# Performance work log

Measured on AMD Instinct MI355X. Metric: run time of the kernel, lower is better.

## Reference

```python
import jax, jax.numpy as jnp
import numpy as np
from jax import lax

D_MODEL = 768
D_INNER = 1536  # expand * dim
D_STATE = 16
D_CONV = 4
DEPTH = 12
IMG = 224
PATCH = 16
BATCH = 8
NUM_PATCHES = ((IMG - PATCH) // PATCH + 1) ** 2  # 196
L = NUM_PATCHES + 1  # 197 (cls token)
EPS = 1e-5


def setup_inputs() -> dict:
    key = jax.random.key(0)
    ks = jax.random.split(key, 16)
    s = 0.02  # trunc_normal std used by the torch module
    conv_std = np.sqrt(2.0 / (PATCH * PATCH * D_MODEL)).astype(np.float32)
    A = jnp.tile(jnp.log(jnp.arange(1, D_STATE + 1, dtype=jnp.float32)), (DEPTH, D_INNER, 1))
    return {
        "x": jax.random.normal(ks[0], (BATCH, 3, IMG, IMG), jnp.float32),
        "conv_w": jax.random.normal(ks[1], (D_MODEL, 3, PATCH, PATCH), jnp.float32) * conv_std,
        "conv_b": jnp.zeros((D_MODEL,), jnp.float32),
        "cls_token": jax.random.normal(ks[2], (1, 1, D_MODEL), jnp.float32) * s,
        "pos_embed": jax.random.normal(ks[3], (1, L, D_MODEL), jnp.float32) * s,
        "ln_w": jnp.ones((DEPTH, D_MODEL), jnp.float32),
        "ln_b": jnp.zeros((DEPTH, D_MODEL), jnp.float32),
        "in_proj_w": jax.random.normal(ks[4], (DEPTH, 2 * D_INNER, D_MODEL), jnp.float32) * s,
        "conv1d_w": jax.random.normal(ks[5], (DEPTH, D_INNER, 1, D_CONV), jnp.float32) * 0.25,
        "conv1d_b": jnp.zeros((DEPTH, D_INNER), jnp.float32),
        "x_proj_w": jax.random.normal(ks[6], (DEPTH, 2 * D_STATE, D_INNER), jnp.float32) * s,
        "dt_proj_w": jax.random.normal(ks[7], (DEPTH, D_INNER, D_INNER), jnp.float32) * s,
        "dt_proj_b": jnp.zeros((DEPTH, D_INNER), jnp.float32),
        "A_log": A,
        "D_param": jnp.ones((DEPTH, D_INNER), jnp.float32),
        "out_proj_w": jax.random.normal(ks[8], (DEPTH, D_MODEL, D_INNER), jnp.float32) * s,
        "norm_w": jnp.ones((D_MODEL,), jnp.float32),
        "norm_b": jnp.zeros((D_MODEL,), jnp.float32),
    }


def layernorm(x, w, b):
    m = jnp.mean(x, axis=-1, keepdims=True)
    v = jnp.mean(jnp.square(x - m), axis=-1, keepdims=True)
    return (x - m) * lax.rsqrt(v + EPS) * w + b


def mamba_block(x, in_w, cw, cb, xp_w, dt_w, dt_b, A_log, Dp, out_w):
    # x: (B, L, D_MODEL)
    Bn = x.shape[0]
    xz = jnp.einsum("bld,ed->ble", x, in_w)            # (B,L,2*di)
    xi, z = jnp.split(xz, 2, axis=-1)
    # depthwise causal conv1d (torch pads d_conv-1 both sides then truncates to L == left-pad only)
    xc = lax.conv_general_dilated(
        xi.transpose(0, 2, 1), cw, window_strides=(1,), padding=[(D_CONV - 1, 0)],
        dimension_numbers=("NCH", "OIH", "NCH"), feature_group_count=D_INNER)
    xc = (xc + cb[None, :, None]).transpose(0, 2, 1)    # (B,L,di)
    xc = jax.nn.silu(xc)
    x_dbl = jnp.einsum("ble,se->bls", xc, xp_w)         # (B,L,2*ds)
    B_ssm = x_dbl[..., D_STATE:]                        # second chunk only (first is discarded in source)
    delta = jax.nn.softplus(jnp.einsum("ble,fe->blf", xc, dt_w) + dt_b)  # (B,L,di)
    A = -jnp.exp(A_log)                                  # (di,ds)
    deltaA = jnp.exp(delta[..., None] * A)               # (B,L,di,ds)
    dBx = (delta * xc)[..., None] * B_ssm[:, :, None, :]  # (B,L,di,ds)

    def step(s, inp):
        dA_t, t_t, b_t = inp                             # (B,di,ds),(B,di,ds),(B,ds)
        s = dA_t * s + t_t
        y = jnp.sum(s * b_t[:, None, :], axis=-1)        # (B,di)
        return s, y

    s0 = jnp.zeros((Bn, D_INNER, D_STATE), x.dtype)
    _, ys = lax.scan(step, s0, (deltaA.transpose(1, 0, 2, 3),
                                dBx.transpose(1, 0, 2, 3),
                                B_ssm.transpose(1, 0, 2)))
    y = ys.transpose(1, 0, 2) + Dp * xc                  # (B,L,di)
    y = y * jax.nn.silu(z)
    return jnp.einsum("ble,de->bld", y, out_w)


def reference(x, conv_w, conv_b, cls_token, pos_embed, ln_w, ln_b, in_proj_w,
              conv1d_w, conv1d_b, x_proj_w, dt_proj_w, dt_proj_b, A_log,
              D_param, out_proj_w, norm_w, norm_b):
    Bn = x.shape[0]
    # overlapping patch embed (stride==patch here -> non-overlap)
    p = lax.conv_general_dilated(x, conv_w, (PATCH, PATCH), "VALID",
                                 dimension_numbers=("NCHW", "OIHW", "NCHW"))
    p = p + conv_b[None, :, None, None]
    t = p.reshape(Bn, D_MODEL, -1).transpose(0, 2, 1)    # (B, 196, D)
    cls = jnp.broadcast_to(cls_token, (Bn, 1, D_MODEL))
    t = jnp.concatenate([cls, t], axis=1) + pos_embed    # (B, 197, D)
    for i in range(DEPTH):
        t = t + mamba_block(layernorm(t, ln_w[i], ln_b[i]), in_proj_w[i],
                            conv1d_w[i], conv1d_b[i], x_proj_w[i], dt_proj_w[i],
                            dt_proj_b[i], A_log[i], D_param[i], out_proj_w[i])
    return layernorm(t, norm_w, norm_b)
```

## Files before the change

kernel.cpp:

```cpp
#include <hip/hip_runtime.h>
#include <math.h>

#define D_MODEL 768
#define D_INNER 1536
#define D_STATE 16
#define DEPTH   12
#define LSEQ    197
#define BATCH   8
#define NPATCH  196
#define ROWS    (BATCH*LSEQ)
#define PROWS   (BATCH*NPATCH)
#define MPAD    1664
#define LP      208
#define NDTX    1664

typedef __bf16 bf16x8 __attribute__((ext_vector_type(8)));
typedef float  floatx4 __attribute__((ext_vector_type(4)));
typedef __attribute__((address_space(1))) void gvoid;
typedef __attribute__((address_space(3))) void svoid;

__device__ __forceinline__ float siluf(float x) { return x / (1.f + __expf(-x)); }

__device__ __forceinline__ void gload_lds16(const void* g, void* s) {
  __builtin_amdgcn_global_load_lds((const gvoid*)g, (svoid*)s, 16, 0, 0);
}

template<int CTRL>
__device__ __forceinline__ float dpp_addf(float x) {
  union { float f; int i; } a, b;
  a.f = x;
  b.i = __builtin_amdgcn_update_dpp(0, a.i, CTRL, 0xF, 0xF, true);
  return x + b.f;
}

__global__ void cvt_k(const float* __restrict__ src, __bf16* __restrict__ dst, int n) {
  int i = (blockIdx.x * 256 + threadIdx.x) * 4;
  if (i >= n) return;
  float4 v = *(const float4*)(src + i);
  union { __bf16 h[4]; unsigned long long u; } p;
  p.h[0] = (__bf16)v.x; p.h[1] = (__bf16)v.y; p.h[2] = (__bf16)v.z; p.h[3] = (__bf16)v.w;
  *(unsigned long long*)(dst + i) = p.u;
}

__global__ void cvt_dtx_k(const float* __restrict__ dtw, const float* __restrict__ xpw,
                          __bf16* __restrict__ dst) {
  size_t i = ((size_t)blockIdx.x * 256 + threadIdx.x) * 4;
  const size_t TOT = (size_t)DEPTH * 1552 * 1536;
  if (i >= TOT) return;
  int layer = (int)(i / (1552 * 1536));
  int rem = (int)(i - (size_t)layer * (1552 * 1536));
  int r = rem / 1536, c = rem - r * 1536;
  const float* src = (r < 1536)
      ? dtw + ((size_t)layer * 1536 + r) * 1536 + c
      : xpw + ((size_t)layer * 32 + 16 + (r - 1536)) * 1536 + c;
  float4 v = *(const float4*)src;
  union { __bf16 h[4]; unsigned long long u; } p;
  p.h[0] = (__bf16)v.x; p.h[1] = (__bf16)v.y; p.h[2] = (__bf16)v.z; p.h[3] = (__bf16)v.w;
  *(unsigned long long*)(dst + ((size_t)layer * NDTX + r) * 1536 + c) = p.u;
}

__global__ void im2col_k(const float* __restrict__ x, __bf16* __restrict__ col) {
  int idx = blockIdx.x * 256 + threadIdx.x;
  if (idx >= PROWS * 768) return;
  int row = idx / 768, i = idx % 768;
  int b = row / NPATCH, p = row % NPATCH;
  int py = p / 14, px = p % 14;
  int ci = i >> 8, rem = i & 255;
  int ky = rem >> 4, kx = rem & 15;
  col[idx] = (__bf16)x[(((size_t)b*3 + ci)*224 + (py*16+ky))*224 + (px*16+kx)];
}

__global__ void assemble_k(const float* __restrict__ P, const float* __restrict__ cb,
                           const float* __restrict__ cls, const float* __restrict__ pos,
                           float* __restrict__ t) {
  int bl = blockIdx.x; int b = bl / LSEQ, l = bl % LSEQ;
  for (int c = threadIdx.x; c < 768; c += 256) {
    float v;
    if (l == 0) v = cls[c];
    else        v = P[((size_t)b*NPATCH + (l-1))*768 + c] + cb[c];
    t[(size_t)bl*768 + c] = v + pos[(size_t)l*768 + c];
  }
}

template<typename T, int FUSE>
__global__ void lnf_k(float* __restrict__ t, const float* __restrict__ part,
                      const float* __restrict__ w, const float* __restrict__ b,
                      T* __restrict__ o) {
  int row = blockIdx.x;
  float* tr = t + (size_t)row * 768;
  float v[3]; float s = 0.f, ss = 0.f;
  #pragma unroll
  for (int i = 0; i < 3; i++) {
    int c = threadIdx.x + i*256;
    float x = tr[c];
    if (FUSE) {
      const size_t S = (size_t)ROWS*768, idx = (size_t)row*768 + c;
      x += part[idx] + part[S+idx] + part[2*S+idx] + part[3*S+idx];
      if (FUSE == 1) tr[c] = x;
    }
    v[i] = x; s += x; ss += x*x;
  }
  __shared__ float red[8];
  #pragma unroll
  for (int off = 32; off; off >>= 1) {
    s  += __shfl_down(s, off, 64);
    ss += __shfl_down(ss, off, 64);
  }
  int wv = threadIdx.x >> 6;
  if ((threadIdx.x & 63) == 0) { red[wv] = s; red[wv+4] = ss; }
  __syncthreads();
  if (threadIdx.x == 0) {
    float S = red[0]+red[1]+red[2]+red[3];
    float SS = red[4]+red[5]+red[6]+red[7];
    float m = S * (1.f/768.f);
    float var = SS * (1.f/768.f) - m*m;
    red[0] = m; red[1] = rsqrtf(var + 1e-5f);
  }
  __syncthreads();
  float m = red[0], r = red[1];
  #pragma unroll
  for (int i = 0; i < 3; i++) {
    int c = threadIdx.x + i*256;
    o[(size_t)row*768 + c] = (T)((v[i]-m)*r*w[c] + b[c]);
  }
}

__global__ __launch_bounds__(256) void mgemm3_k(const __bf16* __restrict__ A,
    const __bf16* __restrict__ W, float* __restrict__ C, size_t pstride,
    int M, int N, int K, int Ksub, int combos, int nt) {
  __shared__ __bf16 sA[2][64*64];
  __shared__ __bf16 sB[2][128*64];
  const int lin = blockIdx.x;
  const int nwg = combos * 25;
  const int q = nwg >> 3, r = nwg & 7;
  const int xcd = lin & 7, idx = lin >> 3;
  const int v = (xcd < r ? xcd * (q + 1) : r * (q + 1) + (xcd - r) * q) + idx;
  const int c = v / 25, mt = v - c * 25;
  const int ntile = c % nt, z = c / nt;
  const int m0 = mt * 64, n0 = ntile * 128;
  const int kbeg = z * Ksub, kend = kbeg + Ksub;

  const int tid = threadIdx.x, wave = tid >> 6, lane = tid & 63;
  const int wm = (wave & 1) * 32, wn = (wave >> 1) * 64;

  floatx4 acc[2][4] = {};

  const int srow = tid >> 3;
  const int scol = ((tid & 7) ^ (srow & 7)) * 8;
  const __bf16* gA = A + (size_t)(m0 + srow) * K + scol;
  const __bf16* gB = W + (size_t)(n0 + srow) * K + scol;

  const int lm = lane & 15, lk = lane >> 4;
  const int g0 = ((lk    ) ^ (lane & 7)) * 8;
  const int g1 = ((lk + 4) ^ (lane & 7)) * 8;

  int buf = 0;
  {
    #pragma unroll
    for (int p = 0; p < 2; p++)
      gload_lds16(gA + (size_t)(p*32)*K + kbeg, sA[0] + p*2048 + tid*8);
    #pragma unroll
    for (int p = 0; p < 4; p++)
      gload_lds16(gB + (size_t)(p*32)*K + kbeg, sB[0] + p*2048 + tid*8);
  }

  for (int k0 = kbeg; k0 < kend; k0 += 64) {
    __syncthreads();
    if (k0 + 64 < kend) {
      const int nb = buf ^ 1;
      #pragma unroll
      for (int p = 0; p < 2; p++)
        gload_lds16(gA + (size_t)(p*32)*K + (k0+64), sA[nb] + p*2048 + tid*8);
      #pragma unroll
      for (int p = 0; p < 4; p++)
        gload_lds16(gB + (size_t)(p*32)*K + (k0+64), sB[nb] + p*2048 + tid*8);
    }
    const __bf16* pA = sA[buf] + (wm + lm) * 64;
    const __bf16* pB = sB[buf] + (wn + lm) * 64;
    bf16x8 a0[2], a1[2], b0[4], b1[4];
    #pragma unroll
    for (int i = 0; i < 2; i++) {
      a0[i] = *(const bf16x8*)(pA + i*1024 + g0);
      a1[i] = *(const bf16x8*)(pA + i*1024 + g1);
    }
    #pragma unroll
    for (int j = 0; j < 4; j++) {
      b0[j] = *(const bf16x8*)(pB + j*1024 + g0);
      b1[j] = *(const bf16x8*)(pB + j*1024 + g1);
    }
    #pragma unroll
    for (int i = 0; i < 2; i++)
      #pragma unroll
      for (int j = 0; j < 4; j++) {
        acc[i][j] = __builtin_amdgcn_mfma_f32_16x16x32_bf16(a0[i], b0[j], acc[i][j], 0, 0, 0);
        acc[i][j] = __builtin_amdgcn_mfma_f32_16x16x32_bf16(a1[i], b1[j], acc[i][j], 0, 0, 0);
      }
    buf ^= 1;
  }

  float* Cp = C + (size_t)z * pstride;
  const int en = n0 + wn + lm;
  const int em = m0 + wm + lk * 4;
  #pragma unroll
  for (int i = 0; i < 2; i++) {
    #pragma unroll
    for (int r2 = 0; r2 < 4; r2++) {
      int m = em + i * 16 + r2;
      if (m >= M) continue;
      #pragma unroll
      for (int j = 0; j < 4; j++)
        Cp[(size_t)m * N + en + j * 16] = acc[i][j][r2];
    }
  }
}

__global__ __launch_bounds__(256) void reduce_dtx_k(const float* __restrict__ p0,
    const float* __restrict__ bias, float* __restrict__ dvT, float* __restrict__ BsT) {
  __shared__ float s[32 * 65];
  const float* p1 = p0 + (size_t)ROWS * NDTX;
  const int b = blockIdx.x, yb = blockIdx.y, d0 = yb * 64, l0 = blockIdx.z * 32;
  const int t = threadIdx.x;
  const bool isB = (yb == 24);
  #pragma unroll
  for (int e = 0; e < 8; e++) {
    int idx = e * 256 + t;
    int d = idx & 63, l = idx >> 6;
    float v = 0.f;
    int gl = l0 + l;
    if (gl < LSEQ) {
      size_t row = (size_t)(b * LSEQ + gl) * NDTX + d0 + d;
      v = p0[row] + p1[row];
      if (!isB) {
        v += bias[d0 + d];
        v = (v > 20.f) ? v : log1pf(__expf(v));
      }
    }
    s[l * 65 + d] = v;
  }
  __syncthreads();
  #pragma unroll
  for (int e = 0; e < 8; e++) {
    int idx = e * 256 + t;
    int ll = idx & 31, dd = idx >> 5;
    int gl = l0 + ll;
    if (gl < LP) {
      if (!isB)
        dvT[((size_t)b * D_INNER + d0 + dd) * LP + gl] = s[ll * 65 + dd];
      else if (dd < 16)
        BsT[((size_t)b * 16 + dd) * LP + gl] = s[ll * 65 + dd];
    }
  }
}

__global__ __launch_bounds__(256) void convf_k(const float* __restrict__ xz,
    const float* __restrict__ cw, const float* __restrict__ cb,
    __bf16* __restrict__ xc_b, float* __restrict__ xvT, float* __restrict__ gmT) {
  const int b = blockIdx.x, dc = blockIdx.y, lc = blockIdx.z * 28;
  const int d = dc * 256 + threadIdx.x;
  const int lend = min(lc + 28, LSEQ);
  const float* w = cw + (size_t)d * 4;
  const float w0 = w[0], w1 = w[1], w2 = w[2], w3 = w[3];
  const float bias = cb[d];
  float xm3 = 0.f, xm2 = 0.f, xm1 = 0.f;
  const size_t rowbase = ((size_t)b * LSEQ) * 3072 + d;
  if (lc >= 3) {
    xm3 = xz[rowbase + (size_t)(lc-3)*3072];
    xm2 = xz[rowbase + (size_t)(lc-2)*3072];
    xm1 = xz[rowbase + (size_t)(lc-1)*3072];
  }
  const size_t ch = (size_t)b * D_INNER + d;
  float* pxv = xvT + ch * LP;
  float* pgm = gmT + ch * LP;

  int l = lc;
  for (; l + 3 < lend; l += 4) {
    float4 bxv, bgm;
    #pragma unroll
    for (int qd = 0; qd < 4; qd++) {
      int lq = l + qd;
      float x0 = xz[rowbase + (size_t)lq*3072];
      float zc = xz[rowbase + (size_t)lq*3072 + 1536];
      float cv = w0*xm3 + w1*xm2 + w2*xm1 + w3*x0 + bias;
      xm3 = xm2; xm2 = xm1; xm1 = x0;
      float xc = siluf(cv);
      float gm = siluf(zc);
      (&bxv.x)[qd] = xc; (&bgm.x)[qd] = gm;
      xc_b[((size_t)b*LSEQ + lq)*D_INNER + d] = (__bf16)xc;
    }
    *(float4*)(pxv + l) = bxv;
    *(float4*)(pgm + l) = bgm;
  }
  for (; l < lend; l++) {
    float x0 = xz[rowbase + (size_t)l*3072];
    float zc = xz[rowbase + (size_t)l*3072 + 1536];
    float cv = w0*xm3 + w1*xm2 + w2*xm1 + w3*x0 + bias;
    xm3 = xm2; xm2 = xm1; xm1 = x0;
    float xc = siluf(cv);
    float gm = siluf(zc);
    xc_b[((size_t)b*LSEQ + l)*D_INNER + d] = (__bf16)xc;
    pxv[l] = xc; pgm[l] = gm;
  }
}

__global__ __launch_bounds__(256) void scan3_k(const float* __restrict__ dvT,
    const float* __restrict__ xvT, const float* __restrict__ gmT,
    const float* __restrict__ BsT, const float* __restrict__ A_log,
    const float* __restrict__ Dp, __bf16* __restrict__ y) {
  const int grp = threadIdx.x >> 4, n = threadIdx.x & 15;
  const int ch = blockIdx.x * 16 + grp;
  const int b = ch / D_INNER, d = ch - b * D_INNER;
  const float a = -__expf(A_log[(size_t)d * 16 + n]);
  const float dp = Dp[d];
  const size_t base = (size_t)ch * LP;
  const size_t bnb  = ((size_t)b * 16 + n) * LP;
  const size_t brow = (size_t)b * LSEQ;
  float s = 0.f;
  for (int l0 = 0; l0 < LP; l0 += 16) {
    float dv[16], xv[16], bn[16];
    #pragma unroll
    for (int q = 0; q < 4; q++) {
      *(float4*)(dv + q*4) = *(const float4*)(dvT + base + l0 + q*4);
      *(float4*)(xv + q*4) = *(const float4*)(xvT + base + l0 + q*4);
      *(float4*)(bn + q*4) = *(const float4*)(BsT + bnb  + l0 + q*4);
    }
    float gm = gmT[base + l0 + n];
    float yreg = 0.f, xvn = 0.f;
    #pragma unroll
    for (int j = 0; j < 16; j++) {
      s = __expf(dv[j] * a) * s + (dv[j] * xv[j]) * bn[j];
      float part = s * bn[j];
      part = dpp_addf<0xB1>(part);
      part = dpp_addf<0x4E>(part);
      part = dpp_addf<0x141>(part);
      part = dpp_addf<0x140>(part);
      yreg = (n == j) ? part : yreg;
      xvn  = (n == j) ? xv[j] : xvn;
    }
    int lo = l0 + n;
    if (lo < LSEQ) y[(brow + lo) * D_INNER + d] = (__bf16)((yreg + dp * xvn) * gm);
  }
}

extern "C" void kernel_launch(void* const* d_in, const int* in_sizes, int n_in,
                              void* d_out, int out_size, void* d_ws, size_t ws_size,
                              hipStream_t stream) {
  const float* x         = (const float*)d_in[0];
  const float* conv_w    = (const float*)d_in[1];
  const float* conv_b    = (const float*)d_in[2];
  const float* cls_token = (const float*)d_in[3];
  const float* pos_embed = (const float*)d_in[4];
  const float* ln_w      = (const float*)d_in[5];
  const float* ln_b      = (const float*)d_in[6];
  const float* in_proj_w = (const float*)d_in[7];
  const float* conv1d_w  = (const float*)d_in[8];
  const float* conv1d_b  = (const float*)d_in[9];
  const float* x_proj_w  = (const float*)d_in[10];
  const float* dt_proj_w = (const float*)d_in[11];
  const float* dt_proj_b = (const float*)d_in[12];
  const float* A_log     = (const float*)d_in[13];
  const float* D_param   = (const float*)d_in[14];
  const float* out_proj_w= (const float*)d_in[15];
  const float* norm_w    = (const float*)d_in[16];
  const float* norm_b    = (const float*)d_in[17];

  const int N_IN  = 2*D_INNER*D_MODEL;
  const int N_OUT = D_MODEL*D_INNER;
  const size_t TSZ = (size_t)BATCH * D_INNER * LP * 4;

  char* wsb = (char*)d_ws;
  size_t off = 0;
  float* t     = (float*)(wsb + off); off += (size_t)ROWS*768*4;
  float* xz    = (float*)(wsb + off); off += (size_t)ROWS*3072*4;
  float* BsT   = (float*)(wsb + off); off += (size_t)BATCH*16*LP*4;
  float* dvT   = (float*)(wsb + off); off += TSZ;
  float* xvT   = (float*)(wsb + off); off += TSZ;
  float* gmT   = (float*)(wsb + off); off += TSZ;
  float* part  = (float*)(wsb + off); off += (size_t)2*ROWS*NDTX*4;
  __bf16* xn_b = (__bf16*)(wsb + off); off += (size_t)MPAD*768*2;
  __bf16* xc_b = (__bf16*)(wsb + off); off += (size_t)MPAD*1536*2;
  __bf16* y_b  = (__bf16*)(wsb + off); off += (size_t)MPAD*1536*2;
  __bf16* col_b= (__bf16*)(wsb + off); off += (size_t)MPAD*768*2;
  __bf16* cw_b = (__bf16*)(wsb + off); off += (size_t)768*768*2;
  __bf16* wb_in  = (__bf16*)(wsb + off); off += (size_t)DEPTH*N_IN*2;
  __bf16* wb_dtx = (__bf16*)(wsb + off); off += (size_t)DEPTH*NDTX*1536*2;
  __bf16* wb_out = (__bf16*)(wsb + off); off += (size_t)DEPTH*N_OUT*2;

  cvt_k<<<(768*768/4 + 255)/256, 256, 0, stream>>>(conv_w, cw_b, 768*768);
  cvt_k<<<(DEPTH*N_IN/4 + 255)/256, 256, 0, stream>>>(in_proj_w, wb_in, DEPTH*N_IN);
  cvt_dtx_k<<<(DEPTH*1552*1536/4 + 255)/256, 256, 0, stream>>>(dt_proj_w, x_proj_w, wb_dtx);
  cvt_k<<<(DEPTH*N_OUT/4 + 255)/256, 256, 0, stream>>>(out_proj_w, wb_out, DEPTH*N_OUT);

  float* P = xz;
  im2col_k<<<(PROWS*768 + 255)/256, 256, 0, stream>>>(x, col_b);
  mgemm3_k<<<25*6, 256, 0, stream>>>(col_b, cw_b, P, 0, PROWS, 768, 768, 768, 6, 6);
  assemble_k<<<ROWS, 256, 0, stream>>>(P, conv_b, cls_token, pos_embed, t);

  lnf_k<__bf16,0><<<ROWS, 256, 0, stream>>>(t, nullptr, ln_w, ln_b, xn_b);

  for (int i = 0; i < DEPTH; i++) {
    mgemm3_k<<<25*24, 256, 0, stream>>>(xn_b, wb_in + (size_t)i*N_IN, xz, 0,
                                        ROWS, 3072, 768, 768, 24, 24);
    convf_k<<<dim3(8, 6, 8), 256, 0, stream>>>(xz, conv1d_w + (size_t)i*D_INNER*4,
        conv1d_b + (size_t)i*D_INNER, xc_b, xvT, gmT);
    mgemm3_k<<<25*26, 256, 0, stream>>>(xc_b, wb_dtx + (size_t)i*NDTX*1536, part,
        (size_t)ROWS*NDTX, ROWS, NDTX, 1536, 768, 26, 13);
    reduce_dtx_k<<<dim3(8, 25, 7), 256, 0, stream>>>(part,
        dt_proj_b + (size_t)i*D_INNER, dvT, BsT);
    scan3_k<<<(BATCH*D_INNER)/16, 256, 0, stream>>>(dvT, xvT, gmT, BsT,
        A_log + (size_t)i*D_INNER*D_STATE, D_param + (size_t)i*D_INNER, y_b);
    mgemm3_k<<<25*24, 256, 0, stream>>>(y_b, wb_out + (size_t)i*N_OUT, part,
        (size_t)ROWS*768, ROWS, 768, 1536, 384, 24, 6);
    if (i < DEPTH-1)
      lnf_k<__bf16,1><<<ROWS, 256, 0, stream>>>(t, part,
          ln_w + (size_t)(i+1)*768, ln_b + (size_t)(i+1)*768, xn_b);
    else
      lnf_k<float,2><<<ROWS, 256, 0, stream>>>(t, part, norm_w, norm_b, (float*)d_out);
  }
}
```

Measured before the change: 1.770 ms.

## Fuse split-K reduction, softplus, conv and gating into the selective scan kernel

Removes the reduce_dtx kernel and the transposed fp32 dvT/xvT/gmT/BsT intermediates. The scan kernel now reads the two split-K partials, xz and the conv weights directly, recomputes the causal conv, softplus and silu gate per 16-step chunk, and transposes through shared memory. This saves a launch and several full-size fp32 global round trips. In exchange the scan does redundant conv work, reads B rows once per channel group, and adds three block barriers per chunk.

Result: faster. 1.615 ms (-8.8%).

```diff
diff --git a/kernel.cpp b/kernel.cpp
--- a/kernel.cpp
+++ b/kernel.cpp
@@ -20,6 +20,9 @@
 typedef __attribute__((address_space(3))) void svoid;
 
 __device__ __forceinline__ float siluf(float x) { return x / (1.f + __expf(-x)); }
+__device__ __forceinline__ float softplusf(float v) {
+  return (v > 20.f) ? v : log1pf(__expf(v));
+}
 
 __device__ __forceinline__ void gload_lds16(const void* g, void* s) {
   __builtin_amdgcn_global_load_lds((const gvoid*)g, (svoid*)s, 16, 0, 0);
@@ -214,47 +217,9 @@
   }
 }
 
-__global__ __launch_bounds__(256) void reduce_dtx_k(const float* __restrict__ p0,
-    const float* __restrict__ bias, float* __restrict__ dvT, float* __restrict__ BsT) {
-  __shared__ float s[32 * 65];
-  const float* p1 = p0 + (size_t)ROWS * NDTX;
-  const int b = blockIdx.x, yb = blockIdx.y, d0 = yb * 64, l0 = blockIdx.z * 32;
-  const int t = threadIdx.x;
-  const bool isB = (yb == 24);
-  #pragma unroll
-  for (int e = 0; e < 8; e++) {
-    int idx = e * 256 + t;
-    int d = idx & 63, l = idx >> 6;
-    float v = 0.f;
-    int gl = l0 + l;
-    if (gl < LSEQ) {
-      size_t row = (size_t)(b * LSEQ + gl) * NDTX + d0 + d;
-      v = p0[row] + p1[row];
-      if (!isB) {
-        v += bias[d0 + d];
-        v = (v > 20.f) ? v : log1pf(__expf(v));
-      }
-    }
-    s[l * 65 + d] = v;
-  }
-  __syncthreads();
-  #pragma unroll
-  for (int e = 0; e < 8; e++) {
-    int idx = e * 256 + t;
-    int ll = idx & 31, dd = idx >> 5;
-    int gl = l0 + ll;
-    if (gl < LP) {
-      if (!isB)
-        dvT[((size_t)b * D_INNER + d0 + dd) * LP + gl] = s[ll * 65 + dd];
-      else if (dd < 16)
-        BsT[((size_t)b * 16 + dd) * LP + gl] = s[ll * 65 + dd];
-    }
-  }
-}
-
 __global__ __launch_bounds__(256) void convf_k(const float* __restrict__ xz,
     const float* __restrict__ cw, const float* __restrict__ cb,
-    __bf16* __restrict__ xc_b, float* __restrict__ xvT, float* __restrict__ gmT) {
+    __bf16* __restrict__ xc_b) {
   const int b = blockIdx.x, dc = blockIdx.y, lc = blockIdx.z * 28;
   const int d = dc * 256 + threadIdx.x;
   const int lend = min(lc + 28, LSEQ);
@@ -268,62 +233,78 @@
     xm2 = xz[rowbase + (size_t)(lc-2)*3072];
     xm1 = xz[rowbase + (size_t)(lc-1)*3072];
   }
-  const size_t ch = (size_t)b * D_INNER + d;
-  float* pxv = xvT + ch * LP;
-  float* pgm = gmT + ch * LP;
-
-  int l = lc;
-  for (; l + 3 < lend; l += 4) {
-    float4 bxv, bgm;
-    #pragma unroll
-    for (int qd = 0; qd < 4; qd++) {
-      int lq = l + qd;
-      float x0 = xz[rowbase + (size_t)lq*3072];
-      float zc = xz[rowbase + (size_t)lq*3072 + 1536];
-      float cv = w0*xm3 + w1*xm2 + w2*xm1 + w3*x0 + bias;
-      xm3 = xm2; xm2 = xm1; xm1 = x0;
-      float xc = siluf(cv);
-      float gm = siluf(zc);
-      (&bxv.x)[qd] = xc; (&bgm.x)[qd] = gm;
-      xc_b[((size_t)b*LSEQ + lq)*D_INNER + d] = (__bf16)xc;
-    }
-    *(float4*)(pxv + l) = bxv;
-    *(float4*)(pgm + l) = bgm;
-  }
-  for (; l < lend; l++) {
+  for (int l = lc; l < lend; l++) {
     float x0 = xz[rowbase + (size_t)l*3072];
-    float zc = xz[rowbase + (size_t)l*3072 + 1536];
     float cv = w0*xm3 + w1*xm2 + w2*xm1 + w3*x0 + bias;
     xm3 = xm2; xm2 = xm1; xm1 = x0;
-    float xc = siluf(cv);
-    float gm = siluf(zc);
-    xc_b[((size_t)b*LSEQ + l)*D_INNER + d] = (__bf16)xc;
-    pxv[l] = xc; pgm[l] = gm;
-  }
-}
-
-__global__ __launch_bounds__(256) void scan3_k(const float* __restrict__ dvT,
-    const float* __restrict__ xvT, const float* __restrict__ gmT,
-    const float* __restrict__ BsT, const float* __restrict__ A_log,
-    const float* __restrict__ Dp, __bf16* __restrict__ y) {
-  const int grp = threadIdx.x >> 4, n = threadIdx.x & 15;
-  const int ch = blockIdx.x * 16 + grp;
-  const int b = ch / D_INNER, d = ch - b * D_INNER;
-  const float a = -__expf(A_log[(size_t)d * 16 + n]);
-  const float dp = Dp[d];
-  const size_t base = (size_t)ch * LP;
-  const size_t bnb  = ((size_t)b * 16 + n) * LP;
-  const size_t brow = (size_t)b * LSEQ;
+    xc_b[((size_t)b*LSEQ + l)*D_INNER + d] = (__bf16)siluf(cv);
+  }
+}
+
+__global__ __launch_bounds__(256) void scan4_k(const float* __restrict__ p0,
+    const float* __restrict__ xz, const float* __restrict__ dt_bias,
+    const float* __restrict__ cw, const float* __restrict__ cb,
+    const float* __restrict__ A_log, const float* __restrict__ Dp,
+    __bf16* __restrict__ y) {
+  __shared__ __align__(16) float sx[19*16];
+  __shared__ __align__(16) float sdv[16*20];
+  __shared__ __align__(16) float sbn[16*20];
+  __shared__ __align__(16) float sxc[16*20];
+  __shared__ __align__(16) float sgm[16*20];
+
+  const float* p1 = p0 + (size_t)ROWS * NDTX;
+  const int t = threadIdx.x;
+  const int b = blockIdx.x / 96;
+  const int d0 = (blockIdx.x - b * 96) * 16;
+  const int lrow = t >> 4, dl = t & 15;
+  const int grp = t >> 4, n = t & 15;
+
+  const float* wp = cw + (size_t)(d0 + dl) * 4;
+  const float w0 = wp[0], w1 = wp[1], w2 = wp[2], w3 = wp[3];
+  const float cbias  = cb[d0 + dl];
+  const float spbias = dt_bias[d0 + dl];
+  const float a  = -__expf(A_log[(size_t)(d0 + grp) * 16 + n]);
+  const float dp = Dp[d0 + grp];
+
+  const size_t browf = (size_t)b * LSEQ;
   float s = 0.f;
+
   for (int l0 = 0; l0 < LP; l0 += 16) {
+    int gl = l0 + lrow;
+    float pdv = 0.f, pbn = 0.f, zv = 0.f, xval = 0.f;
+    if (gl < LSEQ) {
+      size_t row = browf + gl;
+      size_t pr = row * NDTX;
+      pdv = p0[pr + d0 + dl] + p1[pr + d0 + dl] + spbias;
+      pbn = p0[pr + 1536 + dl] + p1[pr + 1536 + dl];
+      size_t xr = row * 3072;
+      zv   = xz[xr + 1536 + d0 + dl];
+      xval = xz[xr + d0 + dl];
+    }
+    sx[(lrow + 3) * 16 + dl] = xval;
+    if (t < 48) {
+      int hl = t >> 4, hdl = t & 15;
+      int gh = l0 - 3 + hl;
+      float hv = 0.f;
+      if (gh >= 0) hv = xz[(browf + gh) * 3072 + d0 + hdl];
+      sx[hl * 16 + hdl] = hv;
+    }
+    __syncthreads();
+    float xc = w0 * sx[lrow*16 + dl] + w1 * sx[(lrow+1)*16 + dl]
+             + w2 * sx[(lrow+2)*16 + dl] + w3 * sx[(lrow+3)*16 + dl] + cbias;
+    sxc[dl*20 + lrow] = siluf(xc);
+    sdv[dl*20 + lrow] = (gl < LSEQ) ? softplusf(pdv) : 0.f;
+    sbn[dl*20 + lrow] = pbn;
+    sgm[dl*20 + lrow] = siluf(zv);
+    __syncthreads();
     float dv[16], xv[16], bn[16];
     #pragma unroll
     for (int q = 0; q < 4; q++) {
-      *(float4*)(dv + q*4) = *(const float4*)(dvT + base + l0 + q*4);
-      *(float4*)(xv + q*4) = *(const float4*)(xvT + base + l0 + q*4);
-      *(float4*)(bn + q*4) = *(const float4*)(BsT + bnb  + l0 + q*4);
-    }
-    float gm = gmT[base + l0 + n];
+      *(floatx4*)(dv + q*4) = *(const floatx4*)(sdv + grp*20 + q*4);
+      *(floatx4*)(xv + q*4) = *(const floatx4*)(sxc + grp*20 + q*4);
+      *(floatx4*)(bn + q*4) = *(const floatx4*)(sbn + n*20   + q*4);
+    }
+    float gm = sgm[grp*20 + n];
     float yreg = 0.f, xvn = 0.f;
     #pragma unroll
     for (int j = 0; j < 16; j++) {
@@ -337,7 +318,9 @@
       xvn  = (n == j) ? xv[j] : xvn;
     }
     int lo = l0 + n;
-    if (lo < LSEQ) y[(brow + lo) * D_INNER + d] = (__bf16)((yreg + dp * xvn) * gm);
+    if (lo < LSEQ)
+      y[(browf + lo) * D_INNER + d0 + grp] = (__bf16)((yreg + dp * xvn) * gm);
+    __syncthreads();
   }
 }
 
@@ -365,16 +348,11 @@
 
   const int N_IN  = 2*D_INNER*D_MODEL;
   const int N_OUT = D_MODEL*D_INNER;
-  const size_t TSZ = (size_t)BATCH * D_INNER * LP * 4;
 
   char* wsb = (char*)d_ws;
   size_t off = 0;
   float* t     = (float*)(wsb + off); off += (size_t)ROWS*768*4;
   float* xz    = (float*)(wsb + off); off += (size_t)ROWS*3072*4;
-  float* BsT   = (float*)(wsb + off); off += (size_t)BATCH*16*LP*4;
-  float* dvT   = (float*)(wsb + off); off += TSZ;
-  float* xvT   = (float*)(wsb + off); off += TSZ;
-  float* gmT   = (float*)(wsb + off); off += TSZ;
   float* part  = (float*)(wsb + off); off += (size_t)2*ROWS*NDTX*4;
   __bf16* xn_b = (__bf16*)(wsb + off); off += (size_t)MPAD*768*2;
   __bf16* xc_b = (__bf16*)(wsb + off); off += (size_t)MPAD*1536*2;
@@ -401,13 +379,13 @@
     mgemm3_k<<<25*24, 256, 0, stream>>>(xn_b, wb_in + (size_t)i*N_IN, xz, 0,
                                         ROWS, 3072, 768, 768, 24, 24);
     convf_k<<<dim3(8, 6, 8), 256, 0, stream>>>(xz, conv1d_w + (size_t)i*D_INNER*4,
-        conv1d_b + (size_t)i*D_INNER, xc_b, xvT, gmT);
+        conv1d_b + (size_t)i*D_INNER, xc_b);
     mgemm3_k<<<25*26, 256, 0, stream>>>(xc_b, wb_dtx + (size_t)i*NDTX*1536, part,
         (size_t)ROWS*NDTX, ROWS, NDTX, 1536, 768, 26, 13);
-    reduce_dtx_k<<<dim3(8, 25, 7), 256, 0, stream>>>(part,
-        dt_proj_b + (size_t)i*D_INNER, dvT, BsT);
-    scan3_k<<<(BATCH*D_INNER)/16, 256, 0, stream>>>(dvT, xvT, gmT, BsT,
-        A_log + (size_t)i*D_INNER*D_STATE, D_param + (size_t)i*D_INNER, y_b);
+    scan4_k<<<(BATCH*D_INNER)/16, 256, 0, stream>>>(part, xz,
+        dt_proj_b + (size_t)i*D_INNER, conv1d_w + (size_t)i*D_INNER*4,
+        conv1d_b + (size_t)i*D_INNER, A_log + (size_t)i*D_INNER*D_STATE,
+        D_param + (size_t)i*D_INNER, y_b);
     mgemm3_k<<<25*24, 256, 0, stream>>>(y_b, wb_out + (size_t)i*N_OUT, part,
         (size_t)ROWS*768, ROWS, 768, 1536, 384, 24, 6);
     if (i < DEPTH-1)
```
